# Kernel tuning notes

Hardware: AMD Instinct MI355X
Metric: run time of the kernel (lower is better)

Reference implementation:

```python
import jax, jax.numpy as jnp
import numpy as np
from jax import lax

ROUTING_ITERS = 3
EPS = 1e-8


def _conv(x, w, b, stride=1):
    # x: [B,C,H,W], w: [O,C,kh,kw]  (VALID padding, NCHW/OIHW)
    y = lax.conv_general_dilated(x, w, (stride, stride), 'VALID',
                                 dimension_numbers=('NCHW', 'OIHW', 'NCHW'))
    return y + b[None, :, None, None]


def _maxpool2(x):
    return lax.reduce_window(x, -jnp.inf, lax.max, (1, 1, 2, 2), (1, 1, 2, 2), 'VALID')


def _squash(s, axis=-1):
    n2 = jnp.sum(s * s, axis=axis, keepdims=True)
    return s * (n2 / (1.0 + n2)) / jnp.sqrt(n2 + EPS)


def setup_inputs() -> dict:
    key = jax.random.key(0)
    ks = jax.random.split(key, 9)
    p = lambda k, shp: (jax.random.normal(k, shp, dtype=jnp.float32) * 0.05)
    return {
        'x':  jax.random.normal(ks[0], (64, 1, 92, 92), dtype=jnp.float32),
        'w1': p(ks[1], (128, 1, 9, 9)),   'b1': jnp.zeros((128,), jnp.float32),
        'w2': p(ks[2], (64, 128, 5, 5)),  'b2': jnp.zeros((64,), jnp.float32),
        'wc': p(ks[3], (128, 64, 8, 8)),  'bc': jnp.zeros((128,), jnp.float32),
        # routing transform: [num_primary=1024, num_sar=10, out_dim=16, in_dim=32]
        'Wr': p(ks[4], (1024, 10, 16, 32)),
    }


def reference(x, w1, b1, w2, b2, wc, bc, Wr):
    B = x.shape[0]
    # feature extractor (dropout is identity at inference)
    h = jax.nn.relu(_conv(x, w1, b1))          # [B,128,84,84]
    h = _maxpool2(h)                            # [B,128,42,42]
    h = _conv(h, w2, b2)                        # [B,64,38,38]
    # primary capsule conv
    h = _conv(h, wc, bc, stride=2)              # [B,128,16,16]
    # 128 channels = 4 capsule types * 32-dim capsules, 16x16 spatial -> 1024 caps
    u = h.reshape(B, 4, 32, 16, 16).transpose(0, 1, 3, 4, 2).reshape(B, 1024, 32)
    u = _squash(u)                              # [B,1024,32]
    # u_hat: predictions of each primary cap for each SAR cap
    u_hat = jnp.einsum('bpi,ptoi->bpto', u, Wr)  # [B,1024,10,16]
    # dynamic routing
    b_log = jnp.zeros((B, 1024, 10), dtype=x.dtype)
    for _ in range(ROUTING_ITERS):
        c = jax.nn.softmax(b_log, axis=2)               # [B,1024,10]
        s = jnp.einsum('bpt,bpto->bto', c, u_hat)       # [B,10,16]
        v = _squash(s)                                   # [B,10,16]
        b_log = b_log + jnp.einsum('bpto,bto->bpt', u_hat, v)
    likelihood = jnp.sqrt(jnp.sum(v * v, axis=-1) + EPS)  # [B,10]
    return likelihood
```

## Files before the change

kernel.cpp:

```cpp
#include <hip/hip_runtime.h>
#include <hip/hip_bf16.h>
#include <math.h>


#define EPSF 1e-8f

typedef __bf16 bf16x8 __attribute__((ext_vector_type(8)));
typedef __bf16 bf16x4 __attribute__((ext_vector_type(4)));
typedef float floatx4 __attribute__((ext_vector_type(4)));
typedef float floatx16 __attribute__((ext_vector_type(16)));

__global__ __launch_bounds__(256) void k_t_all(const float* __restrict__ Wr,
                                               const float* __restrict__ wc,
                                               const float* __restrict__ w2,
                                               const float* __restrict__ w1,
                                               __bf16* __restrict__ wrb,
                                               __bf16* __restrict__ wca,
                                               __bf16* __restrict__ w2a,
                                               __bf16* __restrict__ w1b) {
    int i = blockIdx.x * 256 + threadIdx.x;
    if (i < 5242880) {
        wrb[i] = (__bf16)Wr[i];
        return;
    }
    int i2 = i - 5242880;
    if (i2 < 524288) {
        int j = i2 & 7, lane = (i2 >> 3) & 63, f = i2 >> 9;
        int ct = f & 3, ks = (f >> 2) & 1, khw = (f >> 3) & 63, icc = f >> 9;
        int c32 = lane & 31, h = lane >> 5;
        int oc = ct * 32 + c32;
        int ic = icc * 32 + ks * 16 + h * 8 + j;
        wca[i2] = (__bf16)wc[(oc * 64 + ic) * 64 + khw];
        return;
    }
    int i3 = i2 - 524288;
    if (i3 < 204800) {
        int j = i3 & 7, lane = (i3 >> 3) & 63, f = i3 >> 9;
        int mt = f & 1, ks = (f >> 1) & 3, rem = f >> 3;
        int khw = rem % 25, icc = rem / 25;
        int c32 = lane & 31, h = lane >> 5;
        int oc = mt * 32 + c32;
        int ic = icc * 64 + ks * 16 + h * 8 + j;
        w2a[i3] = (__bf16)w2[(oc * 128 + ic) * 25 + khw];
        return;
    }
    int i4 = i3 - 204800;
    if (i4 < 12288) {
        int kt = i4 >> 10, oc = (i4 >> 3) & 127, j = i4 & 7;
        int k = kt * 8 + j;
        w1b[i4] = (__bf16)(k < 81 ? w1[oc * 81 + k] : 0.f);
    }
}

__global__ __launch_bounds__(256, 3) void k_conv1_mfma(const float* __restrict__ x,
                                                       const __bf16* __restrict__ w1b,
                                                       const float* __restrict__ b1,
                                                       __bf16* __restrict__ h1n) {
    __shared__ float xs[960];
    __shared__ __bf16 Bl[18432];
    int py = blockIdx.x, b = blockIdx.y;
    int t = threadIdx.x;
    int lane = t & 63, w = t >> 6;
    int cc = lane & 15, q = lane >> 4;

    const float* xb = x + (size_t)b * 8464 + 2 * py * 92;
    for (int j = t; j < 920; j += 256) xs[j] = xb[j];

    bf16x8 af2[2][3];
#pragma unroll
    for (int g2 = 0; g2 < 2; ++g2)
#pragma unroll
        for (int ks = 0; ks < 3; ++ks)
            af2[g2][ks] = *(const bf16x8*)(w1b + ((ks * 4 + q) * 128 + g2 * 64 + w * 16 + cc) * 8);

    __syncthreads();

    if (t < 192) {
        int row = t / 96, pos = t - (t / 96) * 96;
        int sbase = row * 92 + pos;
        bool pvalid = pos < 84;
#pragma unroll
        for (int kt = 0; kt < 12; ++kt) {
            bf16x8 pk;
#pragma unroll
            for (int j = 0; j < 8; ++j) {
                int k = kt * 8 + j;
                int kh = k / 9, kw = k - kh * 9;
                float v = (pvalid && k < 81) ? xs[sbase + kh * 92 + kw] : 0.f;
                pk[j] = (__bf16)v;
            }
            *(bf16x8*)(Bl + ((kt * 2 + row) * 96 + pos) * 8) = pk;
        }
    }
    __syncthreads();

    floatx4 acc[2][2][6];
#pragma unroll
    for (int g2 = 0; g2 < 2; ++g2)
#pragma unroll
        for (int rr = 0; rr < 2; ++rr)
#pragma unroll
            for (int n6 = 0; n6 < 6; ++n6)
                acc[g2][rr][n6] = (floatx4){0.f, 0.f, 0.f, 0.f};

    const char* Bb = (const char*)Bl + cc * 16 + q * 3072;
#pragma unroll
    for (int rr = 0; rr < 2; ++rr)
#pragma unroll
        for (int n6 = 0; n6 < 6; ++n6) {
#pragma unroll
            for (int ks = 0; ks < 3; ++ks) {
                bf16x8 bf = *(const bf16x8*)(Bb + ks * 12288 + rr * 1536 + n6 * 256);
                acc[0][rr][n6] = __builtin_amdgcn_mfma_f32_16x16x32_bf16(af2[0][ks], bf, acc[0][rr][n6], 0, 0, 0);
                acc[1][rr][n6] = __builtin_amdgcn_mfma_f32_16x16x32_bf16(af2[1][ks], bf, acc[1][rr][n6], 0, 0, 0);
            }
        }

#pragma unroll
    for (int g2 = 0; g2 < 2; ++g2) {
        int oc0 = g2 * 64 + w * 16 + q * 4;
        float4 bv = *(const float4*)(b1 + oc0);
        size_t obase = (((size_t)b * 42 + py) * 42) * 128 + oc0;
#pragma unroll
        for (int n6 = 0; n6 < 6; ++n6) {
            bf16x4 pk;
#pragma unroll
            for (int r = 0; r < 4; ++r) {
                float vert = fmaxf(acc[g2][0][n6][r], acc[g2][1][n6][r]);
                float hz = fmaxf(vert, __shfl_xor(vert, 1, 64));
                float pooled = fmaxf(hz + ((const float*)&bv)[r], 0.f);
                pk[r] = (__bf16)pooled;
            }
            if ((cc & 1) == 0) {
                int px = n6 * 8 + (cc >> 1);
                if (px < 42)
                    *(bf16x4*)(h1n + obase + (size_t)px * 128) = pk;
            }
        }
    }
}

__global__ __launch_bounds__(256) void k_conv2(const __bf16* __restrict__ h1n,
                                               const __bf16* __restrict__ w2a,
                                               float* __restrict__ p01) {
    __shared__ __bf16 ins[25704];
    int g = blockIdx.x, b = blockIdx.y, icc = blockIdx.z;
    int row0 = g * 5;
    int t = threadIdx.x;
    int lane = t & 63, w = t >> 6;
    int c32 = lane & 31, h = lane >> 5;
    int validp = (g < 7) ? 190 : 114;
    int ic0 = icc * 64;

    int baseN[2], posi[2];
#pragma unroll
    for (int nt = 0; nt < 2; ++nt) {
        int pi = (w * 2 + nt) * 32 + c32;
        int pc = pi < validp ? pi : validp - 1;
        int r = pc / 38, c = pc - r * 38;
        posi[nt] = pi;
        baseN[nt] = (r * 42 + c) * 136 + h * 16;
    }

#pragma unroll
    for (int half = 0; half < 2; ++half) {
        uint4 rb[6];
        int lo[6];
#pragma unroll
        for (int k = 0; k < 6; ++k) {
            int j = (half * 6 + k) * 256 + t;
            if (j > 3023) j -= 256;
            int lr = j / 336, rem = j - lr * 336;
            int ix = rem >> 3, sb = rem & 7;
            int rg = row0 + lr; if (rg > 41) rg = 41;
            rb[k] = *(const uint4*)(h1n + ((((size_t)b * 42 + rg) * 42 + ix) * 128 + ic0 + sb * 8));
            lo[k] = (lr * 42 + ix) * 136 + sb * 16;
        }
#pragma unroll
        for (int k = 0; k < 6; ++k)
            *(uint4*)((char*)ins + lo[k]) = rb[k];
    }

    floatx16 acc[2][2];
#pragma unroll
    for (int mt = 0; mt < 2; ++mt)
#pragma unroll
        for (int nt = 0; nt < 2; ++nt)
#pragma unroll
            for (int i = 0; i < 16; ++i) acc[mt][nt][i] = 0.f;

    const __bf16* wic = w2a + (size_t)icc * 25 * 4096 + (lane << 3);

    bf16x8 abuf[3][8];
#pragma unroll
    for (int ks = 0; ks < 4; ++ks) {
        abuf[0][ks * 2]     = *(const bf16x8*)(wic + 0 * 4096 + ks * 1024);
        abuf[0][ks * 2 + 1] = *(const bf16x8*)(wic + 0 * 4096 + ks * 1024 + 512);
        abuf[1][ks * 2]     = *(const bf16x8*)(wic + 1 * 4096 + ks * 1024);
        abuf[1][ks * 2 + 1] = *(const bf16x8*)(wic + 1 * 4096 + ks * 1024 + 512);
    }

    __syncthreads();
#pragma unroll
    for (int khw = 0; khw < 25; ++khw) {
        if (khw + 2 < 25) {
            const __bf16* wk2 = wic + (khw + 2) * 4096;
#pragma unroll
            for (int ks = 0; ks < 4; ++ks) {
                abuf[(khw + 2) % 3][ks * 2]     = *(const bf16x8*)(wk2 + ks * 1024);
                abuf[(khw + 2) % 3][ks * 2 + 1] = *(const bf16x8*)(wk2 + ks * 1024 + 512);
            }
        }
        int kh = khw / 5, kw = khw - kh * 5;
        int doff = (kh * 42 + kw) * 136;
#pragma unroll
        for (int ks = 0; ks < 4; ++ks) {
            bf16x8 a0 = abuf[khw % 3][ks * 2];
            bf16x8 a1 = abuf[khw % 3][ks * 2 + 1];
#pragma unroll
            for (int nt = 0; nt < 2; ++nt) {
                bf16x8 bfr = *(const bf16x8*)((char*)ins + baseN[nt] + doff + ks * 32);
                acc[0][nt] = __builtin_amdgcn_mfma_f32_32x32x16_bf16(a0, bfr, acc[0][nt], 0, 0, 0);
                acc[1][nt] = __builtin_amdgcn_mfma_f32_32x32x16_bf16(a1, bfr, acc[1][nt], 0, 0, 0);
            }
        }
    }
    float* pdst = p01 + (size_t)icc * 5914624;
#pragma unroll
    for (int nt = 0; nt < 2; ++nt) {
        int pi = posi[nt];
        if (pi < validp) {
            int r = pi / 38, c = pi - r * 38;
            int oh = row0 + r;
            size_t obase = (((size_t)b * 38 + oh) * 38 + c) * 64;
#pragma unroll
            for (int mt = 0; mt < 2; ++mt) {
#pragma unroll
                for (int g2 = 0; g2 < 4; ++g2) {
                    int oc0 = mt * 32 + g2 * 8 + h * 4;
                    floatx4 pv;
                    pv[0] = acc[mt][nt][g2 * 4 + 0];
                    pv[1] = acc[mt][nt][g2 * 4 + 1];
                    pv[2] = acc[mt][nt][g2 * 4 + 2];
                    pv[3] = acc[mt][nt][g2 * 4 + 3];
                    *(floatx4*)(pdst + obase + oc0) = pv;
                }
            }
        }
    }
}

__global__ __launch_bounds__(256) void k_reduce_h2(const float* __restrict__ p01,
                                                   const float* __restrict__ b2,
                                                   __bf16* __restrict__ h2n) {
    int i = blockIdx.x * 256 + threadIdx.x;
    if (i >= 1478656) return;
    size_t e = (size_t)i * 4;
    floatx4 a = *(const floatx4*)(p01 + e);
    floatx4 b = *(const floatx4*)(p01 + 5914624 + e);
    floatx4 bv = *(const floatx4*)(b2 + ((i * 4) & 63));
    bf16x4 pk;
    pk.x = (__bf16)(a[0] + b[0] + bv[0]);
    pk.y = (__bf16)(a[1] + b[1] + bv[1]);
    pk.z = (__bf16)(a[2] + b[2] + bv[2]);
    pk.w = (__bf16)(a[3] + b[3] + bv[3]);
    *(bf16x4*)(h2n + e) = pk;
}

__global__ __launch_bounds__(256, 4) void k_convcaps(const __bf16* __restrict__ h2n,
                                                     const __bf16* __restrict__ wca,
                                                     float* __restrict__ pc) {
    __shared__ __bf16 ins[13680];
    int g = blockIdx.x, b = blockIdx.y, icc = blockIdx.z;
    int t = threadIdx.x;
    int lane = t & 63, ct = t >> 6;
    int c32 = lane & 31, h = lane >> 5;
    int rloc = c32 >> 4, cx = c32 & 15;
    int ic0 = icc * 32;

    floatx16 acc;
#pragma unroll
    for (int i = 0; i < 16; ++i) acc[i] = 0.f;

    int Bbase = (76 * rloc + cx) * 72 + h * 16;
    {
        uint4 rb[6];
        int lo[6];
#pragma unroll
        for (int k = 0; k < 6; ++k) {
            int j = k * 256 + t;
            if (j > 1519) j -= 256;
            int r = j / 152, rem = j - r * 152;
            int c = rem >> 2, s = rem & 3;
            rb[k] = *(const uint4*)(h2n + ((((size_t)b * 38 + 4 * g + r) * 38 + c) * 64 + ic0 + s * 8));
            int X = (r * 2 + (c & 1)) * 19 + (c >> 1);
            lo[k] = X * 72 + s * 16;
        }
#pragma unroll
        for (int k = 0; k < 6; ++k)
            *(uint4*)((char*)ins + lo[k]) = rb[k];
    }
    __syncthreads();
    const __bf16* wic = wca + ((size_t)icc * 64 * 8 + ct) * 512 + (lane << 3);
#pragma unroll
    for (int khw = 0; khw < 64; ++khw) {
        int kh = khw >> 3, kw = khw & 7;
        int par = kw & 1, k2 = kw >> 1;
        int doff = ((kh * 2 + par) * 19 + k2) * 72;
        const __bf16* wk = wic + khw * 4096;
#pragma unroll
        for (int ks = 0; ks < 2; ++ks) {
            bf16x8 af = *(const bf16x8*)(wk + ks * 2048);
            bf16x8 bfr = *(const bf16x8*)((char*)ins + Bbase + doff + ks * 32);
            acc = __builtin_amdgcn_mfma_f32_32x32x16_bf16(af, bfr, acc, 0, 0, 0);
        }
    }
    int pos = (2 * g + rloc) * 16 + cx;
    float* dst = pc + (size_t)icc * 2097152 + (((size_t)b * 1024 + ct * 256 + pos) * 32);
#pragma unroll
    for (int g2 = 0; g2 < 4; ++g2) {
        floatx4 pv;
        pv[0] = acc[g2 * 4 + 0];
        pv[1] = acc[g2 * 4 + 1];
        pv[2] = acc[g2 * 4 + 2];
        pv[3] = acc[g2 * 4 + 3];
        *(floatx4*)(dst + g2 * 8 + h * 4) = pv;
    }
}

__global__ __launch_bounds__(256) void k_squash(const float* __restrict__ pc,
                                                const float* __restrict__ bc,
                                                __bf16* __restrict__ ub) {
    int i = blockIdx.x * 256 + threadIdx.x;
    if (i >= 65536) return;
    int ct = (i >> 8) & 3;
    const float* p0 = pc + (size_t)i * 32;
    const float* p1 = pc + 2097152 + (size_t)i * 32;
    const float* bv = bc + ct * 32;
    float vals[32];
    float n2 = 0.f;
#pragma unroll
    for (int k = 0; k < 8; ++k) {
        floatx4 a = *(const floatx4*)(p0 + k * 4);
        floatx4 b = *(const floatx4*)(p1 + k * 4);
        floatx4 bb = *(const floatx4*)(bv + k * 4);
#pragma unroll
        for (int e = 0; e < 4; ++e) {
            float v = a[e] + b[e] + bb[e];
            vals[k * 4 + e] = v;
            n2 = fmaf(v, v, n2);
        }
    }
    float scale = (n2 / (1.f + n2)) / sqrtf(n2 + EPSF);
    __bf16* dst = ub + (size_t)i * 32;
#pragma unroll
    for (int k = 0; k < 8; ++k) {
        bf16x4 pk;
        pk.x = (__bf16)(vals[k * 4 + 0] * scale);
        pk.y = (__bf16)(vals[k * 4 + 1] * scale);
        pk.z = (__bf16)(vals[k * 4 + 2] * scale);
        pk.w = (__bf16)(vals[k * 4 + 3] * scale);
        *(bf16x4*)(dst + k * 4) = pk;
    }
}

__global__ __launch_bounds__(256, 2) void k_uhat(const __bf16* __restrict__ ub,
                                                 const __bf16* __restrict__ wrb,
                                                 __bf16* __restrict__ uhT) {
    int pt = blockIdx.x, ts = blockIdx.y, bz = blockIdx.z;
    int t = threadIdx.x;
    int p = pt * 64 + (t & 63);
    int q = t >> 6;
    bf16x8 wf[4][4];
#pragma unroll
    for (int o4 = 0; o4 < 4; ++o4)
#pragma unroll
        for (int j = 0; j < 4; ++j)
            wf[o4][j] = *(const bf16x8*)(wrb + (((size_t)p * 10 + ts) * 16 + q * 4 + o4) * 32 + j * 8);
#pragma unroll 1
    for (int bi = 0; bi < 16; ++bi) {
        int b = bz * 16 + bi;
        bf16x8 uf[4];
        const bf16x8* up = (const bf16x8*)(ub + ((size_t)b * 1024 + p) * 32);
#pragma unroll
        for (int j = 0; j < 4; ++j) uf[j] = up[j];
#pragma unroll
        for (int o4 = 0; o4 < 4; ++o4) {
            float s = 0.f;
#pragma unroll
            for (int j = 0; j < 4; ++j)
#pragma unroll
                for (int e = 0; e < 8; ++e)
                    s = fmaf((float)uf[j][e], (float)wf[o4][j][e], s);
            uhT[(((size_t)b * 10 + ts) * 16 + q * 4 + o4) * 1024 + p] = (__bf16)s;
        }
    }
}

__global__ __launch_bounds__(256) void k_route(const __bf16* __restrict__ uhT,
                                               const float* __restrict__ blR,
                                               float* __restrict__ blW,
                                               float* __restrict__ out,
                                               int first, int dob, int last) {
    __shared__ __bf16 uh_s[16384];
    __shared__ float sred[4][16];
    __shared__ float vs[16];
    int b = blockIdx.x, tt = blockIdx.y;
    int t = threadIdx.x;
    const __bf16* uhb = uhT + ((size_t)b * 10 + tt) * 16384;
#pragma unroll
    for (int k = 0; k < 8; ++k) {
        int j = k * 256 + t;
        *(uint4*)((char*)uh_s + j * 16) = *(const uint4*)((const char*)uhb + j * 16);
    }
    __syncthreads();

    float acc[16];
#pragma unroll
    for (int o = 0; o < 16; ++o) acc[o] = 0.f;
    const float* blb = blR + b * 10240;
    for (int p = t; p < 1024; p += 256) {
        float c;
        if (first) {
            c = 0.1f;
        } else {
            float den = 0.f, et = 0.f;
#pragma unroll
            for (int tp = 0; tp < 10; ++tp) {
                float e = expf(blb[tp * 1024 + p]);
                den += e;
                if (tp == tt) et = e;
            }
            c = et / den;
        }
#pragma unroll
        for (int o = 0; o < 16; ++o)
            acc[o] = fmaf(c, (float)uh_s[o * 1024 + p], acc[o]);
    }
    int lane = t & 63, wid = t >> 6;
#pragma unroll
    for (int o = 0; o < 16; ++o) {
        float v = acc[o];
#pragma unroll
        for (int off = 32; off >= 1; off >>= 1) v += __shfl_xor(v, off, 64);
        if (lane == 0) sred[wid][o] = v;
    }
    __syncthreads();
    if (t < 16) {
        float s = (sred[0][t] + sred[1][t]) + (sred[2][t] + sred[3][t]);
        float n2 = s * s;
#pragma unroll
        for (int off = 1; off < 16; off <<= 1) n2 += __shfl_xor(n2, off, 16);
        float scale = (n2 / (1.f + n2)) / sqrtf(n2 + EPSF);
        vs[t] = s * scale;
        if (last && t == 0) {
            float sv2 = n2 * scale * scale;
            out[b * 10 + tt] = sqrtf(sv2 + EPSF);
        }
    }
    __syncthreads();

    if (dob) {
        const float* blr = blR + (b * 10 + tt) * 1024;
        float* blw = blW + (b * 10 + tt) * 1024;
        for (int p = t; p < 1024; p += 256) {
            float d = 0.f;
#pragma unroll
            for (int o = 0; o < 16; ++o) d = fmaf((float)uh_s[o * 1024 + p], vs[o], d);
            blw[p] = first ? d : (blr[p] + d);
        }
    }
}

extern "C" void kernel_launch(void* const* d_in, const int* in_sizes, int n_in,
                              void* d_out, int out_size, void* d_ws, size_t ws_size,
                              hipStream_t stream) {
    const float* x  = (const float*)d_in[0];
    const float* w1 = (const float*)d_in[1];
    const float* b1 = (const float*)d_in[2];
    const float* w2 = (const float*)d_in[3];
    const float* b2 = (const float*)d_in[4];
    const float* wc = (const float*)d_in[5];
    const float* bc = (const float*)d_in[6];
    const float* Wr = (const float*)d_in[7];
    float* out = (float*)d_out;
    float* ws  = (float*)d_ws;

    __bf16* w2a = (__bf16*)(ws);
    __bf16* wca = (__bf16*)(ws + 102400);
    __bf16* w1b = (__bf16*)(ws + 364544);
    __bf16* h1n = (__bf16*)(ws + 375040);
    __bf16* h2n = (__bf16*)(ws + 7600384);
    __bf16* ub  = (__bf16*)(ws + 12654848);
    float*  blA = ws + 14752000;
    __bf16* wrb = (__bf16*)(ws + 15417600);
    float*  p01 = ws + 18039040;
    float*  pc  = ws + 18039040;
    float*  blB = ws + 29868288;
    __bf16* uhT = (__bf16*)(ws + 375040);

    k_t_all<<<23376, 256, 0, stream>>>(Wr, wc, w2, w1, wrb, wca, w2a, w1b);
    k_conv1_mfma<<<dim3(42, 64), 256, 0, stream>>>(x, w1b, b1, h1n);
    k_conv2<<<dim3(8, 64, 2), 256, 0, stream>>>(h1n, w2a, p01);
    k_reduce_h2<<<5776, 256, 0, stream>>>(p01, b2, h2n);
    k_convcaps<<<dim3(8, 64, 2), 256, 0, stream>>>(h2n, wca, pc);
    k_squash<<<256, 256, 0, stream>>>(pc, bc, ub);
    k_uhat<<<dim3(16, 10, 4), 256, 0, stream>>>(ub, wrb, uhT);
    k_route<<<dim3(64, 10), 256, 0, stream>>>(uhT, blA, blA, out, 1, 1, 0);
    k_route<<<dim3(64, 10), 256, 0, stream>>>(uhT, blA, blB, out, 0, 1, 0);
    k_route<<<dim3(64, 10), 256, 0, stream>>>(uhT, blB, blB, out, 0, 0, 1);
}
```

Before: 282.4 us.

## Stage conv2 weights in LDS and drop the idle fourth wave

The conv2 kernel now runs with 192 threads (three waves) instead of 256. The fourth wave previously mapped to output positions beyond the 190 valid ones and did mostly redundant work. Weight slices for three kernel taps at a time are copied cooperatively into a new shared-memory buffer, replacing the per-wave register-prefetched global weight loads. This cuts duplicate global/L2 weight traffic across waves. In exchange it adds about 24KB of LDS, two block barriers per chunk with no double buffering, and it exposes the weight load latency at each chunk boundary.

```diff
diff --git a/kernel.cpp b/kernel.cpp
--- a/kernel.cpp
+++ b/kernel.cpp
@@ -140,10 +140,11 @@
     }
 }
 
-__global__ __launch_bounds__(256) void k_conv2(const __bf16* __restrict__ h1n,
-                                               const __bf16* __restrict__ w2a,
-                                               float* __restrict__ p01) {
+__global__ __launch_bounds__(192, 2) void k_conv2(const __bf16* __restrict__ h1n,
+                                                  const __bf16* __restrict__ w2a,
+                                                  float* __restrict__ p01) {
     __shared__ __bf16 ins[25704];
+    __shared__ __bf16 wsl[12288];
     int g = blockIdx.x, b = blockIdx.y, icc = blockIdx.z;
     int row0 = g * 5;
     int t = threadIdx.x;
@@ -164,12 +165,12 @@
 
 #pragma unroll
     for (int half = 0; half < 2; ++half) {
-        uint4 rb[6];
-        int lo[6];
-#pragma unroll
-        for (int k = 0; k < 6; ++k) {
-            int j = (half * 6 + k) * 256 + t;
-            if (j > 3023) j -= 256;
+        uint4 rb[8];
+        int lo[8];
+#pragma unroll
+        for (int k = 0; k < 8; ++k) {
+            int j = (half * 8 + k) * 192 + t;
+            if (j > 3023) j -= 192;
             int lr = j / 336, rem = j - lr * 336;
             int ix = rem >> 3, sb = rem & 7;
             int rg = row0 + lr; if (rg > 41) rg = 41;
@@ -177,7 +178,7 @@
             lo[k] = (lr * 42 + ix) * 136 + sb * 16;
         }
 #pragma unroll
-        for (int k = 0; k < 6; ++k)
+        for (int k = 0; k < 8; ++k)
             *(uint4*)((char*)ins + lo[k]) = rb[k];
     }
 
@@ -189,42 +190,38 @@
 #pragma unroll
             for (int i = 0; i < 16; ++i) acc[mt][nt][i] = 0.f;
 
-    const __bf16* wic = w2a + (size_t)icc * 25 * 4096 + (lane << 3);
-
-    bf16x8 abuf[3][8];
-#pragma unroll
-    for (int ks = 0; ks < 4; ++ks) {
-        abuf[0][ks * 2]     = *(const bf16x8*)(wic + 0 * 4096 + ks * 1024);
-        abuf[0][ks * 2 + 1] = *(const bf16x8*)(wic + 0 * 4096 + ks * 1024 + 512);
-        abuf[1][ks * 2]     = *(const bf16x8*)(wic + 1 * 4096 + ks * 1024);
-        abuf[1][ks * 2 + 1] = *(const bf16x8*)(wic + 1 * 4096 + ks * 1024 + 512);
-    }
-
-    __syncthreads();
-#pragma unroll
-    for (int khw = 0; khw < 25; ++khw) {
-        if (khw + 2 < 25) {
-            const __bf16* wk2 = wic + (khw + 2) * 4096;
+    const __bf16* wbase = w2a + (size_t)icc * 102400;
+    int laneoff = lane << 3;
+
+#pragma unroll
+    for (int ch = 0; ch < 9; ++ch) {
+        const int k0 = ch * 3;
+        const int nk = (ch == 8) ? 1 : 3;
+        __syncthreads();
+        const uint4* src = (const uint4*)(wbase + k0 * 4096);
+        for (int j = t; j < nk * 512; j += 192)
+            *(uint4*)((char*)wsl + j * 16) = src[j];
+        __syncthreads();
+#pragma unroll
+        for (int kk = 0; kk < nk; ++kk) {
+            int khw = k0 + kk;
+            int kh = khw / 5, kw = khw - kh * 5;
+            int doff = (kh * 42 + kw) * 136;
+            const __bf16* wk = wsl + kk * 4096 + laneoff;
 #pragma unroll
             for (int ks = 0; ks < 4; ++ks) {
-                abuf[(khw + 2) % 3][ks * 2]     = *(const bf16x8*)(wk2 + ks * 1024);
-                abuf[(khw + 2) % 3][ks * 2 + 1] = *(const bf16x8*)(wk2 + ks * 1024 + 512);
-            }
-        }
-        int kh = khw / 5, kw = khw - kh * 5;
-        int doff = (kh * 42 + kw) * 136;
-#pragma unroll
-        for (int ks = 0; ks < 4; ++ks) {
-            bf16x8 a0 = abuf[khw % 3][ks * 2];
-            bf16x8 a1 = abuf[khw % 3][ks * 2 + 1];
-#pragma unroll
-            for (int nt = 0; nt < 2; ++nt) {
-                bf16x8 bfr = *(const bf16x8*)((char*)ins + baseN[nt] + doff + ks * 32);
-                acc[0][nt] = __builtin_amdgcn_mfma_f32_32x32x16_bf16(a0, bfr, acc[0][nt], 0, 0, 0);
-                acc[1][nt] = __builtin_amdgcn_mfma_f32_32x32x16_bf16(a1, bfr, acc[1][nt], 0, 0, 0);
-            }
-        }
-    }
+                bf16x8 a0 = *(const bf16x8*)(wk + ks * 1024);
+                bf16x8 a1 = *(const bf16x8*)(wk + ks * 1024 + 512);
+#pragma unroll
+                for (int nt = 0; nt < 2; ++nt) {
+                    bf16x8 bfr = *(const bf16x8*)((char*)ins + baseN[nt] + doff + ks * 32);
+                    acc[0][nt] = __builtin_amdgcn_mfma_f32_32x32x16_bf16(a0, bfr, acc[0][nt], 0, 0, 0);
+                    acc[1][nt] = __builtin_amdgcn_mfma_f32_32x32x16_bf16(a1, bfr, acc[1][nt], 0, 0, 0);
+                }
+            }
+        }
+    }
+
     float* pdst = p01 + (size_t)icc * 5914624;
 #pragma unroll
     for (int nt = 0; nt < 2; ++nt) {
@@ -501,7 +498,7 @@
 
     k_t_all<<<23376, 256, 0, stream>>>(Wr, wc, w2, w1, wrb, wca, w2a, w1b);
     k_conv1_mfma<<<dim3(42, 64), 256, 0, stream>>>(x, w1b, b1, h1n);
-    k_conv2<<<dim3(8, 64, 2), 256, 0, stream>>>(h1n, w2a, p01);
+    k_conv2<<<dim3(8, 64, 2), 192, 0, stream>>>(h1n, w2a, p01);
     k_reduce_h2<<<5776, 256, 0, stream>>>(p01, b2, h2n);
     k_convcaps<<<dim3(8, 64, 2), 256, 0, stream>>>(h2n, wca, pc);
     k_squash<<<256, 256, 0, stream>>>(pc, bc, ub);
```

After: 282.6 us. About the same (+0.1%).
